# Performance work log

Hardware: AMD Instinct MI355X
Metric: run time of the kernel (lower is better)

Reference implementation:

```python
import jax, jax.numpy as jnp
import numpy as np

N = 100000   # nodes
E = 1600000  # edges (avg degree 16)
F_IN = 128
HID = 128
C_OUT = 10
BN_EPS = 1e-5


def setup_inputs() -> dict:
    key = jax.random.key(0)
    ks = jax.random.split(key, 20)
    x = jax.random.normal(ks[0], (N, F_IN), jnp.float32)
    src = jax.random.randint(ks[1], (E,), 0, N)
    dst = jax.random.randint(ks[2], (E,), 0, N)
    def lin(k, fi, fo):
        return jax.random.normal(k, (fi, fo), jnp.float32) * (1.0 / np.sqrt(fi))
    inp = {
        "x": x, "src": src, "dst": dst,
        "W1": lin(ks[3], F_IN, HID), "b1": jnp.zeros((HID,), jnp.float32),
        "g1": jax.random.normal(ks[4], (HID,), jnp.float32) * 0.1 + 1.0,
        "be1": jax.random.normal(ks[5], (HID,), jnp.float32) * 0.1,
        "m1": jax.random.normal(ks[6], (HID,), jnp.float32) * 0.1,
        "v1": jax.random.uniform(ks[7], (HID,), jnp.float32, 0.5, 1.5),
        "W2": lin(ks[8], HID, HID), "b2": jnp.zeros((HID,), jnp.float32),
        "g2": jax.random.normal(ks[9], (HID,), jnp.float32) * 0.1 + 1.0,
        "be2": jax.random.normal(ks[10], (HID,), jnp.float32) * 0.1,
        "m2": jax.random.normal(ks[11], (HID,), jnp.float32) * 0.1,
        "v2": jax.random.uniform(ks[12], (HID,), jnp.float32, 0.5, 1.5),
        "W3": lin(ks[13], HID, C_OUT), "b3": jnp.zeros((C_OUT,), jnp.float32),
    }
    return inp


def _gcn_conv(x, W, b, src, dst):
    # PyG GCNConv: linear, add self-loops, symmetric deg^-1/2 normalization, scatter-add.
    h = x @ W                                            # [N, out]
    deg = jax.ops.segment_sum(jnp.ones((E,), h.dtype), dst, num_segments=N) + 1.0  # self-loop
    dinv = jax.lax.rsqrt(deg)                            # deg^{-1/2}, [N]
    coef = dinv[src] * dinv[dst]                         # per-edge norm, [E]
    agg = jax.ops.segment_sum(h[src] * coef[:, None], dst, num_segments=N)
    agg = agg + h * (dinv * dinv)[:, None]               # self-loop contribution
    return agg + b


def _bn_eval(x, g, be, m, v):
    return (x - m) * jax.lax.rsqrt(v + BN_EPS) * g + be


def reference(x, src, dst, W1, b1, g1, be1, m1, v1,
              W2, b2, g2, be2, m2, v2, W3, b3):
    h = jax.nn.relu(_bn_eval(_gcn_conv(x, W1, b1, src, dst), g1, be1, m1, v1))
    h = jax.nn.relu(_bn_eval(_gcn_conv(h, W2, b2, src, dst), g2, be2, m2, v2))
    return _gcn_conv(h, W3, b3, src, dst)                # [N, C_OUT] logits
```

## Files before the change

### kernel.cpp

```cpp
#include <hip/hip_runtime.h>

#define NN 100000
#define NE 1600000
#define FD 128
#define CO 10
#define BN_EPS 1e-5f
#define NBUK ((NN + 127) / 128)
#define NBUKP 784
#define BCAP 3072
#define SEGE 4096
#define NSEG ((NE + SEGE - 1) / SEGE)

typedef __attribute__((ext_vector_type(8))) short short8;
typedef __attribute__((ext_vector_type(4))) float f32x4;

__device__ __forceinline__ unsigned short f2bf(float f) {
  unsigned int u = __builtin_bit_cast(unsigned int, f);
  u = (u + 0x7FFFu + ((u >> 16) & 1u)) >> 16;
  return (unsigned short)u;
}
__device__ __forceinline__ float bf2f(unsigned short h) {
  unsigned int u = ((unsigned int)h) << 16;
  return __builtin_bit_cast(float, u);
}
__device__ __forceinline__ float blo(unsigned int u) {
  return __builtin_bit_cast(float, u << 16);
}
__device__ __forceinline__ float bhi(unsigned int u) {
  return __builtin_bit_cast(float, u & 0xFFFF0000u);
}
__device__ __forceinline__ unsigned int cvt_pk_bf16(float a, float b) {
  unsigned int r;
  asm("v_cvt_pk_bf16_f32 %0, %1, %2" : "=v"(r) : "v"(a), "v"(b));
  return r;
}

__global__ __launch_bounds__(256) void k_hist(const int* __restrict__ dst,
                                              int* __restrict__ histM) {
  __shared__ int hist[NBUK];
  int b = blockIdx.x, t = threadIdx.x;
  for (int i = t; i < NBUK; i += 256) hist[i] = 0;
  __syncthreads();
  int e0 = b * SEGE, e1 = min(e0 + SEGE, NE);
  for (int e = e0 + t; e < e1; e += 256) atomicAdd(&hist[dst[e] >> 7], 1);
  __syncthreads();
  for (int i = t; i < NBUK; i += 256) histM[b * NBUKP + i] = hist[i];
}

__global__ __launch_bounds__(256) void k_colscan(const int* __restrict__ histM,
                                                 int* __restrict__ segbase,
                                                 int* __restrict__ btot) {
  __shared__ int lds[256];
  int b = blockIdx.x, t = threadIdx.x;
  int s0 = t * 2, s1 = t * 2 + 1;
  int v0 = (s0 < NSEG) ? histM[s0 * NBUKP + b] : 0;
  int v1 = (s1 < NSEG) ? histM[s1 * NBUKP + b] : 0;
  int pair = v0 + v1;
  lds[t] = pair;
  __syncthreads();
  int mine = pair;
  for (int off = 1; off < 256; off <<= 1) {
    int add = (t >= off) ? lds[t - off] : 0;
    __syncthreads();
    lds[t] += add;
    __syncthreads();
  }
  int run = lds[t] - mine;
  if (s0 < NSEG) segbase[s0 * NBUKP + b] = run;
  if (s1 < NSEG) segbase[s1 * NBUKP + b] = run + v0;
  if (t == 255) btot[b] = lds[255];
}

__global__ __launch_bounds__(256) void k_scatter2(const int* __restrict__ src,
                                                  const int* __restrict__ dst,
                                                  const int* __restrict__ segbase,
                                                  unsigned int* __restrict__ buck) {
  __shared__ int base[NBUK];
  int b = blockIdx.x, t = threadIdx.x;
  for (int i = t; i < NBUK; i += 256) base[i] = segbase[b * NBUKP + i];
  __syncthreads();
  int e0 = b * SEGE, e1 = min(e0 + SEGE, NE);
  for (int e = e0 + t; e < e1; e += 256) {
    int s = src[e], d = dst[e];
    int bk = d >> 7;
    int slot = atomicAdd(&base[bk], 1);
    buck[(size_t)bk * BCAP + slot] = ((unsigned int)(d & 127) << 17) | (unsigned int)s;
  }
}

__global__ __launch_bounds__(256) void k_btotscan(const int* __restrict__ btot,
                                                  int* __restrict__ bbase) {
  __shared__ int lds[256];
  int t = threadIdx.x;
  int v[4];
  int s = 0;
#pragma unroll
  for (int i = 0; i < 4; ++i) {
    int idx = t * 4 + i;
    v[i] = (idx < NBUK) ? btot[idx] : 0;
    s += v[i];
  }
  lds[t] = s;
  __syncthreads();
  int mine = s;
  for (int off = 1; off < 256; off <<= 1) {
    int add = (t >= off) ? lds[t - off] : 0;
    __syncthreads();
    lds[t] += add;
    __syncthreads();
  }
  int run = lds[t] - mine;
#pragma unroll
  for (int i = 0; i < 4; ++i) {
    int idx = t * 4 + i;
    if (idx < NBUK) {
      bbase[idx] = run;
      run += v[i];
    }
  }
}

__global__ __launch_bounds__(256) void k_finalize(const int* __restrict__ btot,
                                                  const int* __restrict__ bbase,
                                                  const unsigned int* __restrict__ buck,
                                                  int* __restrict__ row_start,
                                                  float* __restrict__ dinv,
                                                  int* __restrict__ csr_src) {
  __shared__ unsigned int ebuf[BCAP];
  __shared__ int cnt[128];
  __shared__ int xoff[128];
  int b = blockIdx.x, t = threadIdx.x;
  int nb = btot[b];
  int base = bbase[b];
  const unsigned int* bp = buck + (size_t)b * BCAP;
  for (int i = t; i < nb; i += 256) ebuf[i] = bp[i];
  if (t < 128) cnt[t] = 0;
  __syncthreads();
  for (int i = t; i < nb; i += 256) atomicAdd(&cnt[ebuf[i] >> 17], 1);
  __syncthreads();
  if (t < 128) xoff[t] = cnt[t];
  __syncthreads();
  for (int off = 1; off < 128; off <<= 1) {
    int add = 0;
    if (t < 128 && t >= off) add = xoff[t - off];
    __syncthreads();
    if (t < 128) xoff[t] += add;
    __syncthreads();
  }
  if (t < 128) {
    int node = b * 128 + t;
    int ex = xoff[t] - cnt[t];
    if (node < NN) {
      row_start[node] = base + ex;
      dinv[node] = rsqrtf((float)cnt[t] + 1.0f);
    }
    xoff[t] = ex;
    cnt[t] = 0;
  }
  if (b == 0 && t == 0) row_start[NN] = NE;
  __syncthreads();
  for (int i = t; i < nb; i += 256) {
    unsigned int p = ebuf[i];
    int dl = (int)(p >> 17);
    int l = atomicAdd(&cnt[dl], 1);
    csr_src[base + xoff[dl] + l] = (int)(p & 0x1FFFFu);
  }
}

__global__ __launch_bounds__(256) void k_prep(const float* __restrict__ W1,
                                              const float* __restrict__ W2,
                                              unsigned short* __restrict__ w1hi,
                                              unsigned short* __restrict__ w1lo,
                                              unsigned short* __restrict__ w2hi,
                                              unsigned short* __restrict__ w2lo,
                                              const float* __restrict__ b1, const float* __restrict__ g1,
                                              const float* __restrict__ be1, const float* __restrict__ m1,
                                              const float* __restrict__ v1,
                                              const float* __restrict__ b2, const float* __restrict__ g2,
                                              const float* __restrict__ be2, const float* __restrict__ m2,
                                              const float* __restrict__ v2,
                                              float* __restrict__ sc1, float* __restrict__ sh1,
                                              float* __restrict__ sc2, float* __restrict__ sh2) {
  int b = blockIdx.x, t = threadIdx.x;
  if (b < 128) {
    const float* W = (b < 64) ? W1 : W2;
    unsigned short* whi = (b < 64) ? w1hi : w2hi;
    unsigned short* wlo = (b < 64) ? w1lo : w2lo;
    int i = ((b & 63) * 256 + t);
    int k = i >> 7, n = i & 127;
    float w = W[i];
    unsigned short h = f2bf(w);
    unsigned short l = f2bf(w - bf2f(h));
    int idx = ((((k >> 5) * 8) + (n >> 4)) * 64 + ((k >> 3) & 3) * 16 + (n & 15)) * 8 + (k & 7);
    whi[idx] = h;
    wlo[idx] = l;
  } else {
    if (t < FD) {
      float s = g1[t] * rsqrtf(v1[t] + BN_EPS);
      sc1[t] = s;
      sh1[t] = (b1[t] - m1[t]) * s + be1[t];
    } else if (t < 2 * FD) {
      int f = t - FD;
      float s = g2[f] * rsqrtf(v2[f] + BN_EPS);
      sc2[f] = s;
      sh2[f] = (b2[f] - m2[f]) * s + be2[f];
    }
  }
}

__global__ __launch_bounds__(256) void k_gemm128_mfma(const float* __restrict__ X,
                                                      const unsigned short* __restrict__ whi,
                                                      const unsigned short* __restrict__ wlo,
                                                      const float* __restrict__ dinv,
                                                      unsigned short* __restrict__ Hbs,
                                                      int nrows) {
  int tid = threadIdx.x;
  int lane = tid & 63, wv = tid >> 6;
  int lg = lane >> 4, li = lane & 15;
  int wr0 = blockIdx.x * 64 + wv * 16;
  int row = wr0 + li;
  bool ok = row < nrows;

  short8 ahi[4], alo[4];
#pragma unroll
  for (int ks = 0; ks < 4; ++ks) {
    if (ok) {
      const float* xp = X + (unsigned)(row * FD + ks * 32 + lg * 8);
      float4 v0 = *(const float4*)xp;
      float4 v1 = *(const float4*)(xp + 4);
      float f[8] = {v0.x, v0.y, v0.z, v0.w, v1.x, v1.y, v1.z, v1.w};
      unsigned int hp[4], lp[4];
#pragma unroll
      for (int j = 0; j < 4; ++j) {
        float a = f[2 * j], c = f[2 * j + 1];
        hp[j] = cvt_pk_bf16(a, c);
        float ra = a - blo(hp[j]);
        float rc = c - bhi(hp[j]);
        lp[j] = cvt_pk_bf16(ra, rc);
      }
      uint4 hv = {hp[0], hp[1], hp[2], hp[3]};
      uint4 lv = {lp[0], lp[1], lp[2], lp[3]};
      ahi[ks] = __builtin_bit_cast(short8, hv);
      alo[ks] = __builtin_bit_cast(short8, lv);
    } else {
#pragma unroll
      for (int j = 0; j < 8; ++j) { ahi[ks][j] = 0; alo[ks][j] = 0; }
    }
  }

  int rb = wr0 + lg * 4;
  float dvr[4];
#pragma unroll
  for (int r = 0; r < 4; ++r) dvr[r] = (rb + r < nrows) ? dinv[rb + r] : 0.f;

#pragma unroll
  for (int nt = 0; nt < 8; ++nt) {
    f32x4 acc = {0.f, 0.f, 0.f, 0.f};
#pragma unroll
    for (int ks = 0; ks < 4; ++ks) {
      unsigned int bidx = (unsigned)(((ks * 8 + nt) * 64 + lane) * 8);
      short8 bh = *(const short8*)&whi[bidx];
      short8 bl = *(const short8*)&wlo[bidx];
      acc = __builtin_amdgcn_mfma_f32_16x16x32_bf16(ahi[ks], bh, acc, 0, 0, 0);
      acc = __builtin_amdgcn_mfma_f32_16x16x32_bf16(alo[ks], bh, acc, 0, 0, 0);
      acc = __builtin_amdgcn_mfma_f32_16x16x32_bf16(ahi[ks], bl, acc, 0, 0, 0);
    }
    int col = nt * 16 + li;
#pragma unroll
    for (int r = 0; r < 4; ++r) {
      if (rb + r < nrows)
        Hbs[(unsigned)((rb + r) * FD + col)] = f2bf(acc[r] * dvr[r]);
    }
  }
}

template <bool BN>
__global__ __launch_bounds__(256) void k_gather128(const int* __restrict__ row_start,
                                                   const int* __restrict__ csr_src,
                                                   const float* __restrict__ dinv,
                                                   const unsigned short* __restrict__ Hbs,
                                                   const float* __restrict__ sc,
                                                   const float* __restrict__ sh,
                                                   float* __restrict__ AGG) {
  int node = blockIdx.x * 4 + (threadIdx.x >> 6);
  node = __builtin_amdgcn_readfirstlane(node);
  int lane = threadIdx.x & 63;
  const unsigned int* Hc = (const unsigned int*)Hbs;
  int beg = row_start[node], end = row_start[node + 1];
  float px0 = 0.f, px1 = 0.f, px2 = 0.f, px3 = 0.f;
  float py0 = 0.f, py1 = 0.f, py2 = 0.f, py3 = 0.f;
  {
    unsigned int us = Hc[(unsigned)(node * 64) + lane];
    px0 = blo(us); py0 = bhi(us);
  }
  int e = beg;
  for (; e + 3 < end; e += 4) {
    unsigned int u0 = Hc[((unsigned)csr_src[e + 0] << 6) + lane];
    unsigned int u1 = Hc[((unsigned)csr_src[e + 1] << 6) + lane];
    unsigned int u2 = Hc[((unsigned)csr_src[e + 2] << 6) + lane];
    unsigned int u3 = Hc[((unsigned)csr_src[e + 3] << 6) + lane];
    px0 += blo(u0); py0 += bhi(u0);
    px1 += blo(u1); py1 += bhi(u1);
    px2 += blo(u2); py2 += bhi(u2);
    px3 += blo(u3); py3 += bhi(u3);
  }
  for (; e < end; ++e) {
    unsigned int u0 = Hc[((unsigned)csr_src[e] << 6) + lane];
    px0 += blo(u0); py0 += bhi(u0);
  }
  float dv = dinv[node];
  float accx = ((px0 + px1) + (px2 + px3)) * dv;
  float accy = ((py0 + py1) + (py2 + py3)) * dv;
  if (BN) {
    float scx = sc[lane * 2], scy = sc[lane * 2 + 1];
    float shx = sh[lane * 2], shy = sh[lane * 2 + 1];
    accx = fmaxf(fmaf(accx, scx, shx), 0.f);
    accy = fmaxf(fmaf(accy, scy, shy), 0.f);
  }
  float2 o; o.x = accx; o.y = accy;
  ((float2*)AGG)[(unsigned)(node * 64) + lane] = o;
}

__global__ __launch_bounds__(256) void k_gemm_out(const float* __restrict__ X,
                                                  const float* __restrict__ W3,
                                                  float* __restrict__ H3, int nrows) {
  __shared__ float ws[FD * 16];
  int tid = threadIdx.x;
  for (int i = tid; i < FD * 16; i += 256) {
    int k = i >> 4, c = i & 15;
    ws[i] = (c < CO) ? W3[k * CO + c] : 0.f;
  }
  __syncthreads();
  int grp = tid >> 4;
  int c = tid & 15;
  int r = blockIdx.x * 16 + grp;
  if (r >= nrows) return;
  const float* x = X + (unsigned)(r * FD);
  float acc = 0.f;
#pragma unroll
  for (int k = 0; k < FD; k += 4) {
    float4 xv = *(const float4*)&x[k];
    acc += xv.x * ws[(k + 0) * 16 + c];
    acc += xv.y * ws[(k + 1) * 16 + c];
    acc += xv.z * ws[(k + 2) * 16 + c];
    acc += xv.w * ws[(k + 3) * 16 + c];
  }
  if (c < CO) H3[(unsigned)(r * CO + c)] = acc;
}

__global__ __launch_bounds__(256) void k_gather10(const int* __restrict__ row_start,
                                                  const int* __restrict__ csr_src,
                                                  const float* __restrict__ dinv,
                                                  const float* __restrict__ H3,
                                                  const float* __restrict__ b3,
                                                  float* __restrict__ out) {
  int node = blockIdx.x * 16 + (threadIdx.x >> 4);
  if (node >= NN) return;
  int c = threadIdx.x & 15;
  int beg = row_start[node], end = row_start[node + 1];
  float dv = dinv[node];
  float acc = 0.f;
  if (c < CO) acc = H3[(unsigned)(node * CO + c)] * (dv * dv);
  for (int e = beg; e < end; ++e) {
    int s = csr_src[e];
    float cf = dinv[s] * dv;
    if (c < CO) acc = fmaf(H3[(unsigned)(s * CO + c)], cf, acc);
  }
  if (c < CO) out[(unsigned)(node * CO + c)] = acc + b3[c];
}

extern "C" void kernel_launch(void* const* d_in, const int* in_sizes, int n_in,
                              void* d_out, int out_size, void* d_ws, size_t ws_size,
                              hipStream_t stream) {
  const float* x = (const float*)d_in[0];
  const int* src = (const int*)d_in[1];
  const int* dst = (const int*)d_in[2];
  const float* W1 = (const float*)d_in[3];
  const float* b1 = (const float*)d_in[4];
  const float* g1 = (const float*)d_in[5];
  const float* be1 = (const float*)d_in[6];
  const float* m1 = (const float*)d_in[7];
  const float* v1 = (const float*)d_in[8];
  const float* W2 = (const float*)d_in[9];
  const float* b2 = (const float*)d_in[10];
  const float* g2 = (const float*)d_in[11];
  const float* be2 = (const float*)d_in[12];
  const float* m2 = (const float*)d_in[13];
  const float* v2 = (const float*)d_in[14];
  const float* W3 = (const float*)d_in[15];
  const float* b3 = (const float*)d_in[16];
  float* out = (float*)d_out;

  char* wsb = (char*)d_ws;
  int* row_start = (int*)wsb;                 wsb += (NN + 1) * 4;
  int* histM = (int*)wsb;                     wsb += (size_t)NSEG * NBUKP * 4;
  int* segbase = (int*)wsb;                   wsb += (size_t)NSEG * NBUKP * 4;
  int* btot = (int*)wsb;                      wsb += NBUKP * 4;
  int* bbase = (int*)wsb;                     wsb += NBUKP * 4;
  float* dinv = (float*)wsb;                  wsb += NN * 4;
  float* sc1 = (float*)wsb;                   wsb += FD * 4;
  float* sh1 = (float*)wsb;                   wsb += FD * 4;
  float* sc2 = (float*)wsb;                   wsb += FD * 4;
  float* sh2 = (float*)wsb;                   wsb += FD * 4;
  unsigned short* w1hi = (unsigned short*)wsb; wsb += FD * FD * 2;
  unsigned short* w1lo = (unsigned short*)wsb; wsb += FD * FD * 2;
  unsigned short* w2hi = (unsigned short*)wsb; wsb += FD * FD * 2;
  unsigned short* w2lo = (unsigned short*)wsb; wsb += FD * FD * 2;
  int* csr_src = (int*)wsb;                   wsb += (size_t)NE * 4;
  unsigned int* buck = (unsigned int*)wsb;    wsb += (size_t)NBUK * BCAP * 4;
  float* AGG = (float*)wsb;                   wsb += (size_t)NN * FD * 4;
  unsigned short* Hbs = (unsigned short*)wsb; wsb += (size_t)NN * FD * 2;
  float* H3 = (float*)Hbs;

  k_hist<<<NSEG, 256, 0, stream>>>(dst, histM);
  k_colscan<<<NBUK, 256, 0, stream>>>(histM, segbase, btot);
  k_scatter2<<<NSEG, 256, 0, stream>>>(src, dst, segbase, buck);
  k_btotscan<<<1, 256, 0, stream>>>(btot, bbase);
  k_finalize<<<NBUK, 256, 0, stream>>>(btot, bbase, buck, row_start, dinv, csr_src);
  k_prep<<<129, 256, 0, stream>>>(W1, W2, w1hi, w1lo, w2hi, w2lo,
                                  b1, g1, be1, m1, v1, b2, g2, be2, m2, v2,
                                  sc1, sh1, sc2, sh2);

  int gemm_blocks = (NN + 63) / 64;
  int gat_blocks = (NN + 3) / 4;

  k_gemm128_mfma<<<gemm_blocks, 256, 0, stream>>>(x, w1hi, w1lo, dinv, Hbs, NN);
  k_gather128<true><<<gat_blocks, 256, 0, stream>>>(row_start, csr_src, dinv,
                                                    Hbs, sc1, sh1, AGG);
  k_gemm128_mfma<<<gemm_blocks, 256, 0, stream>>>(AGG, w2hi, w2lo, dinv, Hbs, NN);
  k_gather128<true><<<gat_blocks, 256, 0, stream>>>(row_start, csr_src, dinv,
                                                    Hbs, sc2, sh2, AGG);
  k_gemm_out<<<(NN + 15) / 16, 256, 0, stream>>>(AGG, W3, H3, NN);
  k_gather10<<<(NN + 15) / 16, 256, 0, stream>>>(row_start, csr_src, dinv,
                                                 H3, b3, out);
}
```

Baseline: 357.0 us.

## Fuse layer-3 linear into gather, drop bucket scan, merge prep into histogram kernel

The second aggregation kernel now also applies the W3 projection through a wavefront shuffle reduction and pre-scales by dinv. This removes the separate k_gemm_out pass and the write and read of the 128-wide AGG activations. The global bucket-base scan kernel is gone: the CSR keeps per-bucket padded slots, and each node stores a packed uint4 of start, count and dinv, so gathers need one load instead of three. Weight prep is folded into the histogram launch, cutting two launches, at the cost of a padded CSR layout and heavier per-lane register use in the fused gather.

```diff
diff --git a/kernel.cpp b/kernel.cpp
--- a/kernel.cpp
+++ b/kernel.cpp
@@ -5,11 +5,11 @@
 #define FD 128
 #define CO 10
 #define BN_EPS 1e-5f
-#define NBUK ((NN + 127) / 128)
+#define NBUK 782
 #define NBUKP 784
 #define BCAP 3072
 #define SEGE 4096
-#define NSEG ((NE + SEGE - 1) / SEGE)
+#define NSEG 391
 
 typedef __attribute__((ext_vector_type(8))) short short8;
 typedef __attribute__((ext_vector_type(4))) float f32x4;
@@ -35,158 +35,34 @@
   return r;
 }
 
-__global__ __launch_bounds__(256) void k_hist(const int* __restrict__ dst,
-                                              int* __restrict__ histM) {
+__global__ __launch_bounds__(256) void k_hist_prep(
+    const int* __restrict__ dst, int* __restrict__ histM,
+    const float* __restrict__ W1, const float* __restrict__ W2,
+    unsigned short* __restrict__ w1hi, unsigned short* __restrict__ w1lo,
+    unsigned short* __restrict__ w2hi, unsigned short* __restrict__ w2lo,
+    const float* __restrict__ b1, const float* __restrict__ g1,
+    const float* __restrict__ be1, const float* __restrict__ m1,
+    const float* __restrict__ v1,
+    const float* __restrict__ b2, const float* __restrict__ g2,
+    const float* __restrict__ be2, const float* __restrict__ m2,
+    const float* __restrict__ v2,
+    float* __restrict__ sc1, float* __restrict__ sh1,
+    float* __restrict__ sc2, float* __restrict__ sh2) {
   __shared__ int hist[NBUK];
   int b = blockIdx.x, t = threadIdx.x;
-  for (int i = t; i < NBUK; i += 256) hist[i] = 0;
-  __syncthreads();
-  int e0 = b * SEGE, e1 = min(e0 + SEGE, NE);
-  for (int e = e0 + t; e < e1; e += 256) atomicAdd(&hist[dst[e] >> 7], 1);
-  __syncthreads();
-  for (int i = t; i < NBUK; i += 256) histM[b * NBUKP + i] = hist[i];
-}
-
-__global__ __launch_bounds__(256) void k_colscan(const int* __restrict__ histM,
-                                                 int* __restrict__ segbase,
-                                                 int* __restrict__ btot) {
-  __shared__ int lds[256];
-  int b = blockIdx.x, t = threadIdx.x;
-  int s0 = t * 2, s1 = t * 2 + 1;
-  int v0 = (s0 < NSEG) ? histM[s0 * NBUKP + b] : 0;
-  int v1 = (s1 < NSEG) ? histM[s1 * NBUKP + b] : 0;
-  int pair = v0 + v1;
-  lds[t] = pair;
-  __syncthreads();
-  int mine = pair;
-  for (int off = 1; off < 256; off <<= 1) {
-    int add = (t >= off) ? lds[t - off] : 0;
-    __syncthreads();
-    lds[t] += add;
-    __syncthreads();
-  }
-  int run = lds[t] - mine;
-  if (s0 < NSEG) segbase[s0 * NBUKP + b] = run;
-  if (s1 < NSEG) segbase[s1 * NBUKP + b] = run + v0;
-  if (t == 255) btot[b] = lds[255];
-}
-
-__global__ __launch_bounds__(256) void k_scatter2(const int* __restrict__ src,
-                                                  const int* __restrict__ dst,
-                                                  const int* __restrict__ segbase,
-                                                  unsigned int* __restrict__ buck) {
-  __shared__ int base[NBUK];
-  int b = blockIdx.x, t = threadIdx.x;
-  for (int i = t; i < NBUK; i += 256) base[i] = segbase[b * NBUKP + i];
-  __syncthreads();
-  int e0 = b * SEGE, e1 = min(e0 + SEGE, NE);
-  for (int e = e0 + t; e < e1; e += 256) {
-    int s = src[e], d = dst[e];
-    int bk = d >> 7;
-    int slot = atomicAdd(&base[bk], 1);
-    buck[(size_t)bk * BCAP + slot] = ((unsigned int)(d & 127) << 17) | (unsigned int)s;
-  }
-}
-
-__global__ __launch_bounds__(256) void k_btotscan(const int* __restrict__ btot,
-                                                  int* __restrict__ bbase) {
-  __shared__ int lds[256];
-  int t = threadIdx.x;
-  int v[4];
-  int s = 0;
-#pragma unroll
-  for (int i = 0; i < 4; ++i) {
-    int idx = t * 4 + i;
-    v[i] = (idx < NBUK) ? btot[idx] : 0;
-    s += v[i];
-  }
-  lds[t] = s;
-  __syncthreads();
-  int mine = s;
-  for (int off = 1; off < 256; off <<= 1) {
-    int add = (t >= off) ? lds[t - off] : 0;
-    __syncthreads();
-    lds[t] += add;
-    __syncthreads();
-  }
-  int run = lds[t] - mine;
-#pragma unroll
-  for (int i = 0; i < 4; ++i) {
-    int idx = t * 4 + i;
-    if (idx < NBUK) {
-      bbase[idx] = run;
-      run += v[i];
-    }
-  }
-}
-
-__global__ __launch_bounds__(256) void k_finalize(const int* __restrict__ btot,
-                                                  const int* __restrict__ bbase,
-                                                  const unsigned int* __restrict__ buck,
-                                                  int* __restrict__ row_start,
-                                                  float* __restrict__ dinv,
-                                                  int* __restrict__ csr_src) {
-  __shared__ unsigned int ebuf[BCAP];
-  __shared__ int cnt[128];
-  __shared__ int xoff[128];
-  int b = blockIdx.x, t = threadIdx.x;
-  int nb = btot[b];
-  int base = bbase[b];
-  const unsigned int* bp = buck + (size_t)b * BCAP;
-  for (int i = t; i < nb; i += 256) ebuf[i] = bp[i];
-  if (t < 128) cnt[t] = 0;
-  __syncthreads();
-  for (int i = t; i < nb; i += 256) atomicAdd(&cnt[ebuf[i] >> 17], 1);
-  __syncthreads();
-  if (t < 128) xoff[t] = cnt[t];
-  __syncthreads();
-  for (int off = 1; off < 128; off <<= 1) {
-    int add = 0;
-    if (t < 128 && t >= off) add = xoff[t - off];
-    __syncthreads();
-    if (t < 128) xoff[t] += add;
-    __syncthreads();
-  }
-  if (t < 128) {
-    int node = b * 128 + t;
-    int ex = xoff[t] - cnt[t];
-    if (node < NN) {
-      row_start[node] = base + ex;
-      dinv[node] = rsqrtf((float)cnt[t] + 1.0f);
-    }
-    xoff[t] = ex;
-    cnt[t] = 0;
-  }
-  if (b == 0 && t == 0) row_start[NN] = NE;
-  __syncthreads();
-  for (int i = t; i < nb; i += 256) {
-    unsigned int p = ebuf[i];
-    int dl = (int)(p >> 17);
-    int l = atomicAdd(&cnt[dl], 1);
-    csr_src[base + xoff[dl] + l] = (int)(p & 0x1FFFFu);
-  }
-}
-
-__global__ __launch_bounds__(256) void k_prep(const float* __restrict__ W1,
-                                              const float* __restrict__ W2,
-                                              unsigned short* __restrict__ w1hi,
-                                              unsigned short* __restrict__ w1lo,
-                                              unsigned short* __restrict__ w2hi,
-                                              unsigned short* __restrict__ w2lo,
-                                              const float* __restrict__ b1, const float* __restrict__ g1,
-                                              const float* __restrict__ be1, const float* __restrict__ m1,
-                                              const float* __restrict__ v1,
-                                              const float* __restrict__ b2, const float* __restrict__ g2,
-                                              const float* __restrict__ be2, const float* __restrict__ m2,
-                                              const float* __restrict__ v2,
-                                              float* __restrict__ sc1, float* __restrict__ sh1,
-                                              float* __restrict__ sc2, float* __restrict__ sh2) {
-  int b = blockIdx.x, t = threadIdx.x;
-  if (b < 128) {
-    const float* W = (b < 64) ? W1 : W2;
-    unsigned short* whi = (b < 64) ? w1hi : w2hi;
-    unsigned short* wlo = (b < 64) ? w1lo : w2lo;
-    int i = ((b & 63) * 256 + t);
+  if (b < NSEG) {
+    for (int i = t; i < NBUK; i += 256) hist[i] = 0;
+    __syncthreads();
+    int e0 = b * SEGE, e1 = min(e0 + SEGE, NE);
+    for (int e = e0 + t; e < e1; e += 256) atomicAdd(&hist[dst[e] >> 7], 1);
+    __syncthreads();
+    for (int i = t; i < NBUK; i += 256) histM[b * NBUKP + i] = hist[i];
+  } else if (b < NSEG + 128) {
+    int bb = b - NSEG;
+    const float* W = (bb < 64) ? W1 : W2;
+    unsigned short* whi = (bb < 64) ? w1hi : w2hi;
+    unsigned short* wlo = (bb < 64) ? w1lo : w2lo;
+    int i = (bb & 63) * 256 + t;
     int k = i >> 7, n = i & 127;
     float w = W[i];
     unsigned short h = f2bf(w);
@@ -208,10 +84,99 @@
   }
 }
 
+__global__ __launch_bounds__(256) void k_colscan(const int* __restrict__ histM,
+                                                 int* __restrict__ segbase,
+                                                 int* __restrict__ btot) {
+  __shared__ int lds[256];
+  int b = blockIdx.x, t = threadIdx.x;
+  int s0 = t * 2, s1 = t * 2 + 1;
+  int v0 = (s0 < NSEG) ? histM[s0 * NBUKP + b] : 0;
+  int v1 = (s1 < NSEG) ? histM[s1 * NBUKP + b] : 0;
+  int pair = v0 + v1;
+  lds[t] = pair;
+  __syncthreads();
+  int mine = pair;
+  for (int off = 1; off < 256; off <<= 1) {
+    int add = (t >= off) ? lds[t - off] : 0;
+    __syncthreads();
+    lds[t] += add;
+    __syncthreads();
+  }
+  int run = lds[t] - mine;
+  if (s0 < NSEG) segbase[s0 * NBUKP + b] = run;
+  if (s1 < NSEG) segbase[s1 * NBUKP + b] = run + v0;
+  if (t == 255) btot[b] = lds[255];
+}
+
+__global__ __launch_bounds__(256) void k_scatter2(const int* __restrict__ src,
+                                                  const int* __restrict__ dst,
+                                                  const int* __restrict__ segbase,
+                                                  unsigned int* __restrict__ buck) {
+  __shared__ int base[NBUK];
+  int b = blockIdx.x, t = threadIdx.x;
+  for (int i = t; i < NBUK; i += 256) base[i] = segbase[b * NBUKP + i];
+  __syncthreads();
+  int e0 = b * SEGE, e1 = min(e0 + SEGE, NE);
+  for (int e = e0 + t; e < e1; e += 256) {
+    int s = src[e], d = dst[e];
+    int bk = d >> 7;
+    int slot = atomicAdd(&base[bk], 1);
+    buck[(size_t)bk * BCAP + slot] = ((unsigned int)(d & 127) << 17) | (unsigned int)s;
+  }
+}
+
+__global__ __launch_bounds__(256) void k_finalize(const int* __restrict__ btot,
+                                                  const unsigned int* __restrict__ buck,
+                                                  uint4* __restrict__ nrange,
+                                                  int* __restrict__ csr_src) {
+  __shared__ unsigned int ebuf[BCAP];
+  __shared__ int cnt[128];
+  __shared__ int xoff[128];
+  int b = blockIdx.x, t = threadIdx.x;
+  int nb = btot[b];
+  const unsigned int* bp = buck + (size_t)b * BCAP;
+  for (int i = t; i < nb; i += 256) ebuf[i] = bp[i];
+  if (t < 128) cnt[t] = 0;
+  __syncthreads();
+  for (int i = t; i < nb; i += 256) atomicAdd(&cnt[ebuf[i] >> 17], 1);
+  __syncthreads();
+  if (t < 128) xoff[t] = cnt[t];
+  __syncthreads();
+  for (int off = 1; off < 128; off <<= 1) {
+    int add = 0;
+    if (t < 128 && t >= off) add = xoff[t - off];
+    __syncthreads();
+    if (t < 128) xoff[t] += add;
+    __syncthreads();
+  }
+  if (t < 128) {
+    int node = b * 128 + t;
+    int ex = xoff[t] - cnt[t];
+    if (node < NN) {
+      uint4 nr;
+      nr.x = (unsigned)(b * BCAP + ex);
+      nr.y = (unsigned)cnt[t];
+      nr.z = __builtin_bit_cast(unsigned int, rsqrtf((float)cnt[t] + 1.0f));
+      nr.w = 0;
+      nrange[node] = nr;
+    }
+    xoff[t] = ex;
+    cnt[t] = 0;
+  }
+  __syncthreads();
+  int base = b * BCAP;
+  for (int i = t; i < nb; i += 256) {
+    unsigned int p = ebuf[i];
+    int dl = (int)(p >> 17);
+    int l = atomicAdd(&cnt[dl], 1);
+    csr_src[base + xoff[dl] + l] = (int)(p & 0x1FFFFu);
+  }
+}
+
 __global__ __launch_bounds__(256) void k_gemm128_mfma(const float* __restrict__ X,
                                                       const unsigned short* __restrict__ whi,
                                                       const unsigned short* __restrict__ wlo,
-                                                      const float* __restrict__ dinv,
+                                                      const uint4* __restrict__ nrange,
                                                       unsigned short* __restrict__ Hbs,
                                                       int nrows) {
   int tid = threadIdx.x;
@@ -251,7 +216,8 @@
   int rb = wr0 + lg * 4;
   float dvr[4];
 #pragma unroll
-  for (int r = 0; r < 4; ++r) dvr[r] = (rb + r < nrows) ? dinv[rb + r] : 0.f;
+  for (int r = 0; r < 4; ++r)
+    dvr[r] = (rb + r < nrows) ? __builtin_bit_cast(float, nrange[rb + r].z) : 0.f;
 
 #pragma unroll
   for (int nt = 0; nt < 8; ++nt) {
@@ -274,10 +240,8 @@
   }
 }
 
-template <bool BN>
-__global__ __launch_bounds__(256) void k_gather128(const int* __restrict__ row_start,
+__global__ __launch_bounds__(256) void k_gather128(const uint4* __restrict__ nrange,
                                                    const int* __restrict__ csr_src,
-                                                   const float* __restrict__ dinv,
                                                    const unsigned short* __restrict__ Hbs,
                                                    const float* __restrict__ sc,
                                                    const float* __restrict__ sh,
@@ -286,9 +250,11 @@
   node = __builtin_amdgcn_readfirstlane(node);
   int lane = threadIdx.x & 63;
   const unsigned int* Hc = (const unsigned int*)Hbs;
-  int beg = row_start[node], end = row_start[node + 1];
-  float px0 = 0.f, px1 = 0.f, px2 = 0.f, px3 = 0.f;
-  float py0 = 0.f, py1 = 0.f, py2 = 0.f, py3 = 0.f;
+  uint4 nr = nrange[node];
+  int beg = (int)nr.x, end = (int)(nr.x + nr.y);
+  float dv = __builtin_bit_cast(float, nr.z);
+  float px0, px1 = 0.f, px2 = 0.f, px3 = 0.f;
+  float py0, py1 = 0.f, py2 = 0.f, py3 = 0.f;
   {
     unsigned int us = Hc[(unsigned)(node * 64) + lane];
     px0 = blo(us); py0 = bhi(us);
@@ -308,65 +274,94 @@
     unsigned int u0 = Hc[((unsigned)csr_src[e] << 6) + lane];
     px0 += blo(u0); py0 += bhi(u0);
   }
-  float dv = dinv[node];
   float accx = ((px0 + px1) + (px2 + px3)) * dv;
   float accy = ((py0 + py1) + (py2 + py3)) * dv;
-  if (BN) {
-    float scx = sc[lane * 2], scy = sc[lane * 2 + 1];
-    float shx = sh[lane * 2], shy = sh[lane * 2 + 1];
-    accx = fmaxf(fmaf(accx, scx, shx), 0.f);
-    accy = fmaxf(fmaf(accy, scy, shy), 0.f);
-  }
+  float scx = sc[lane * 2], scy = sc[lane * 2 + 1];
+  float shx = sh[lane * 2], shy = sh[lane * 2 + 1];
+  accx = fmaxf(fmaf(accx, scx, shx), 0.f);
+  accy = fmaxf(fmaf(accy, scy, shy), 0.f);
   float2 o; o.x = accx; o.y = accy;
   ((float2*)AGG)[(unsigned)(node * 64) + lane] = o;
 }
 
-__global__ __launch_bounds__(256) void k_gemm_out(const float* __restrict__ X,
-                                                  const float* __restrict__ W3,
-                                                  float* __restrict__ H3, int nrows) {
-  __shared__ float ws[FD * 16];
-  int tid = threadIdx.x;
-  for (int i = tid; i < FD * 16; i += 256) {
-    int k = i >> 4, c = i & 15;
-    ws[i] = (c < CO) ? W3[k * CO + c] : 0.f;
-  }
-  __syncthreads();
-  int grp = tid >> 4;
-  int c = tid & 15;
-  int r = blockIdx.x * 16 + grp;
-  if (r >= nrows) return;
-  const float* x = X + (unsigned)(r * FD);
-  float acc = 0.f;
-#pragma unroll
-  for (int k = 0; k < FD; k += 4) {
-    float4 xv = *(const float4*)&x[k];
-    acc += xv.x * ws[(k + 0) * 16 + c];
-    acc += xv.y * ws[(k + 1) * 16 + c];
-    acc += xv.z * ws[(k + 2) * 16 + c];
-    acc += xv.w * ws[(k + 3) * 16 + c];
-  }
-  if (c < CO) H3[(unsigned)(r * CO + c)] = acc;
-}
-
-__global__ __launch_bounds__(256) void k_gather10(const int* __restrict__ row_start,
+__global__ __launch_bounds__(256) void k_gather128_out(const uint4* __restrict__ nrange,
+                                                       const int* __restrict__ csr_src,
+                                                       const unsigned short* __restrict__ Hbs,
+                                                       const float* __restrict__ sc,
+                                                       const float* __restrict__ sh,
+                                                       const float* __restrict__ W3,
+                                                       float* __restrict__ H3s) {
+  int node = blockIdx.x * 4 + (threadIdx.x >> 6);
+  node = __builtin_amdgcn_readfirstlane(node);
+  int lane = threadIdx.x & 63;
+  float w3r[20];
+  {
+    const float* wp = W3 + lane * 2 * CO;
+#pragma unroll
+    for (int j = 0; j < 20; ++j) w3r[j] = wp[j];
+  }
+  const unsigned int* Hc = (const unsigned int*)Hbs;
+  uint4 nr = nrange[node];
+  int beg = (int)nr.x, end = (int)(nr.x + nr.y);
+  float dv = __builtin_bit_cast(float, nr.z);
+  float px0, px1 = 0.f, px2 = 0.f, px3 = 0.f;
+  float py0, py1 = 0.f, py2 = 0.f, py3 = 0.f;
+  {
+    unsigned int us = Hc[(unsigned)(node * 64) + lane];
+    px0 = blo(us); py0 = bhi(us);
+  }
+  int e = beg;
+  for (; e + 3 < end; e += 4) {
+    unsigned int u0 = Hc[((unsigned)csr_src[e + 0] << 6) + lane];
+    unsigned int u1 = Hc[((unsigned)csr_src[e + 1] << 6) + lane];
+    unsigned int u2 = Hc[((unsigned)csr_src[e + 2] << 6) + lane];
+    unsigned int u3 = Hc[((unsigned)csr_src[e + 3] << 6) + lane];
+    px0 += blo(u0); py0 += bhi(u0);
+    px1 += blo(u1); py1 += bhi(u1);
+    px2 += blo(u2); py2 += bhi(u2);
+    px3 += blo(u3); py3 += bhi(u3);
+  }
+  for (; e < end; ++e) {
+    unsigned int u0 = Hc[((unsigned)csr_src[e] << 6) + lane];
+    px0 += blo(u0); py0 += bhi(u0);
+  }
+  float accx = ((px0 + px1) + (px2 + px3)) * dv;
+  float accy = ((py0 + py1) + (py2 + py3)) * dv;
+  float scx = sc[lane * 2], scy = sc[lane * 2 + 1];
+  float shx = sh[lane * 2], shy = sh[lane * 2 + 1];
+  accx = fmaxf(fmaf(accx, scx, shx), 0.f);
+  accy = fmaxf(fmaf(accy, scy, shy), 0.f);
+  float p[10];
+#pragma unroll
+  for (int c = 0; c < CO; ++c) p[c] = fmaf(accx, w3r[c], accy * w3r[10 + c]);
+#pragma unroll
+  for (int off = 32; off >= 1; off >>= 1) {
+#pragma unroll
+    for (int c = 0; c < CO; ++c) p[c] += __shfl_xor(p[c], off);
+  }
+#pragma unroll
+  for (int c = 0; c < CO; ++c)
+    if (lane == c) H3s[(unsigned)(node * CO + c)] = p[c] * dv;
+}
+
+__global__ __launch_bounds__(256) void k_gather10(const uint4* __restrict__ nrange,
                                                   const int* __restrict__ csr_src,
-                                                  const float* __restrict__ dinv,
-                                                  const float* __restrict__ H3,
+                                                  const float* __restrict__ H3s,
                                                   const float* __restrict__ b3,
                                                   float* __restrict__ out) {
   int node = blockIdx.x * 16 + (threadIdx.x >> 4);
   if (node >= NN) return;
   int c = threadIdx.x & 15;
-  int beg = row_start[node], end = row_start[node + 1];
-  float dv = dinv[node];
+  uint4 nr = nrange[node];
+  int beg = (int)nr.x, end = (int)(nr.x + nr.y);
+  float dv = __builtin_bit_cast(float, nr.z);
   float acc = 0.f;
-  if (c < CO) acc = H3[(unsigned)(node * CO + c)] * (dv * dv);
+  if (c < CO) acc = H3s[(unsigned)(node * CO + c)];
   for (int e = beg; e < end; ++e) {
     int s = csr_src[e];
-    float cf = dinv[s] * dv;
-    if (c < CO) acc = fmaf(H3[(unsigned)(s * CO + c)], cf, acc);
-  }
-  if (c < CO) out[(unsigned)(node * CO + c)] = acc + b3[c];
+    if (c < CO) acc += H3s[(unsigned)(s * CO + c)];
+  }
+  if (c < CO) out[(unsigned)(node * CO + c)] = fmaf(acc, dv, b3[c]);
 }
 
 extern "C" void kernel_launch(void* const* d_in, const int* in_sizes, int n_in,
@@ -392,45 +387,39 @@
   float* out = (float*)d_out;
 
   char* wsb = (char*)d_ws;
-  int* row_start = (int*)wsb;                 wsb += (NN + 1) * 4;
-  int* histM = (int*)wsb;                     wsb += (size_t)NSEG * NBUKP * 4;
-  int* segbase = (int*)wsb;                   wsb += (size_t)NSEG * NBUKP * 4;
-  int* btot = (int*)wsb;                      wsb += NBUKP * 4;
-  int* bbase = (int*)wsb;                     wsb += NBUKP * 4;
-  float* dinv = (float*)wsb;                  wsb += NN * 4;
-  float* sc1 = (float*)wsb;                   wsb += FD * 4;
-  float* sh1 = (float*)wsb;                   wsb += FD * 4;
-  float* sc2 = (float*)wsb;                   wsb += FD * 4;
-  float* sh2 = (float*)wsb;                   wsb += FD * 4;
+  int* histM = (int*)wsb;                      wsb += (size_t)NSEG * NBUKP * 4;
+  int* segbase = (int*)wsb;                    wsb += (size_t)NSEG * NBUKP * 4;
+  int* btot = (int*)wsb;                       wsb += NBUKP * 4;
+  uint4* nrange = (uint4*)wsb;                 wsb += (size_t)NN * 16;
+  float* sc1 = (float*)wsb;                    wsb += FD * 4;
+  float* sh1 = (float*)wsb;                    wsb += FD * 4;
+  float* sc2 = (float*)wsb;                    wsb += FD * 4;
+  float* sh2 = (float*)wsb;                    wsb += FD * 4;
   unsigned short* w1hi = (unsigned short*)wsb; wsb += FD * FD * 2;
   unsigned short* w1lo = (unsigned short*)wsb; wsb += FD * FD * 2;
   unsigned short* w2hi = (unsigned short*)wsb; wsb += FD * FD * 2;
   unsigned short* w2lo = (unsigned short*)wsb; wsb += FD * FD * 2;
-  int* csr_src = (int*)wsb;                   wsb += (size_t)NE * 4;
-  unsigned int* buck = (unsigned int*)wsb;    wsb += (size_t)NBUK * BCAP * 4;
-  float* AGG = (float*)wsb;                   wsb += (size_t)NN * FD * 4;
-  unsigned short* Hbs = (unsigned short*)wsb; wsb += (size_t)NN * FD * 2;
-  float* H3 = (float*)Hbs;
-
-  k_hist<<<NSEG, 256, 0, stream>>>(dst, histM);
+  int* csr_src = (int*)wsb;                    wsb += (size_t)NBUK * BCAP * 4;
+  unsigned int* buck = (unsigned int*)wsb;     wsb += (size_t)NBUK * BCAP * 4;
+  float* AGG = (float*)wsb;                    wsb += (size_t)NN * FD * 4;
+  unsigned short* Hbs = (unsigned short*)wsb;  wsb += (size_t)NN * FD * 2;
+  float* H3s = (float*)wsb;                    wsb += (size_t)NN * CO * 4;
+
+  k_hist_prep<<<NSEG + 129, 256, 0, stream>>>(dst, histM, W1, W2,
+                                              w1hi, w1lo, w2hi, w2lo,
+                                              b1, g1, be1, m1, v1,
+                                              b2, g2, be2, m2, v2,
+                                              sc1, sh1, sc2, sh2);
   k_colscan<<<NBUK, 256, 0, stream>>>(histM, segbase, btot);
   k_scatter2<<<NSEG, 256, 0, stream>>>(src, dst, segbase, buck);
-  k_btotscan<<<1, 256, 0, stream>>>(btot, bbase);
-  k_finalize<<<NBUK, 256, 0, stream>>>(btot, bbase, buck, row_start, dinv, csr_src);
-  k_prep<<<129, 256, 0, stream>>>(W1, W2, w1hi, w1lo, w2hi, w2lo,
-                                  b1, g1, be1, m1, v1, b2, g2, be2, m2, v2,
-                                  sc1, sh1, sc2, sh2);
+  k_finalize<<<NBUK, 256, 0, stream>>>(btot, buck, nrange, csr_src);
 
   int gemm_blocks = (NN + 63) / 64;
   int gat_blocks = (NN + 3) / 4;
 
-  k_gemm128_mfma<<<gemm_blocks, 256, 0, stream>>>(x, w1hi, w1lo, dinv, Hbs, NN);
-  k_gather128<true><<<gat_blocks, 256, 0, stream>>>(row_start, csr_src, dinv,
-                                                    Hbs, sc1, sh1, AGG);
-  k_gemm128_mfma<<<gemm_blocks, 256, 0, stream>>>(AGG, w2hi, w2lo, dinv, Hbs, NN);
-  k_gather128<true><<<gat_blocks, 256, 0, stream>>>(row_start, csr_src, dinv,
-                                                    Hbs, sc2, sh2, AGG);
-  k_gemm_out<<<(NN + 15) / 16, 256, 0, stream>>>(AGG, W3, H3, NN);
-  k_gather10<<<(NN + 15) / 16, 256, 0, stream>>>(row_start, csr_src, dinv,
-                                                 H3, b3, out);
-}
+  k_gemm128_mfma<<<gemm_blocks, 256, 0, stream>>>(x, w1hi, w1lo, nrange, Hbs, NN);
+  k_gather128<<<gat_blocks, 256, 0, stream>>>(nrange, csr_src, Hbs, sc1, sh1, AGG);
+  k_gemm128_mfma<<<gemm_blocks, 256, 0, stream>>>(AGG, w2hi, w2lo, nrange, Hbs, NN);
+  k_gather128_out<<<gat_blocks, 256, 0, stream>>>(nrange, csr_src, Hbs, sc2, sh2, W3, H3s);
+  k_gather10<<<(NN + 15) / 16, 256, 0, stream>>>(nrange, csr_src, H3s, b3, out);
+}
```

Measured after the change: 313.9 us. -12.1%, faster.
